# Performance work log

Hardware: AMD Instinct MI355X
Metric: run time of the kernel (lower is better)

## Reference

```python
import jax, jax.numpy as jnp
import numpy as np

N = 100000      # nodes
E = 1600000     # edges (before self-loops)
IN_DIM = 128
HEADS1, C1 = 8, 16   # conv1: hidden_dim=16, heads=8 -> 128 concat
OUT_DIM = 40
NEG_SLOPE = 0.2


def setup_inputs() -> dict:
    key = jax.random.key(0)
    ks = jax.random.split(key, 10)
    s = 0.1
    x = jax.random.normal(ks[0], (N, IN_DIM), dtype=jnp.float32)
    edge_index = jax.random.randint(ks[1], (2, E), 0, N)
    W1 = jax.random.normal(ks[2], (IN_DIM, HEADS1 * C1), dtype=jnp.float32) * s
    att_l1 = jax.random.normal(ks[3], (HEADS1, C1), dtype=jnp.float32) * s
    att_r1 = jax.random.normal(ks[4], (HEADS1, C1), dtype=jnp.float32) * s
    b1 = jnp.zeros((HEADS1 * C1,), dtype=jnp.float32)
    W2 = jax.random.normal(ks[5], (HEADS1 * C1, OUT_DIM), dtype=jnp.float32) * s
    att_l2 = jax.random.normal(ks[6], (1, OUT_DIM), dtype=jnp.float32) * s
    att_r2 = jax.random.normal(ks[7], (1, OUT_DIM), dtype=jnp.float32) * s
    b2 = jnp.zeros((OUT_DIM,), dtype=jnp.float32)
    return {"x": x, "edge_index": edge_index, "W1": W1, "att_l1": att_l1,
            "att_r1": att_r1, "b1": b1, "W2": W2, "att_l2": att_l2,
            "att_r2": att_r2, "b2": b2}


def supergat_layer(x, src, dst, W, att_l, att_r, bias, concat):
    """One SuperGATConv layer, MX attention, inference mode (no dropout)."""
    n = x.shape[0]
    heads, out_ch = att_l.shape
    h = (x @ W).reshape(n, heads, out_ch)      # [N, H, C]
    h_i = h[dst]                               # target features  [E2, H, C]
    h_j = h[src]                               # source features  [E2, H, C]
    # MX attention: mix of GO (learned att vectors) gated by DP (dot product)
    logits = jnp.sum(h_i * h_j, axis=-1)                           # [E2, H]
    alpha = jnp.sum(h_j * att_l, axis=-1) + jnp.sum(h_i * att_r, axis=-1)
    alpha = alpha * jax.nn.sigmoid(logits)
    alpha = jax.nn.leaky_relu(alpha, NEG_SLOPE)
    # segment softmax over destination node (every node has a self-loop)
    a_max = jax.ops.segment_max(alpha, dst, num_segments=n)        # [N, H]
    ex = jnp.exp(alpha - a_max[dst])
    denom = jax.ops.segment_sum(ex, dst, num_segments=n)           # [N, H]
    a = ex / denom[dst]                                            # [E2, H]
    out = jax.ops.segment_sum(h_j * a[..., None], dst, num_segments=n)  # [N,H,C]
    if concat:
        out = out.reshape(n, heads * out_ch)
    else:
        out = out.mean(axis=1)
    return out + bias


def reference(x, edge_index, W1, att_l1, att_r1, b1, W2, att_l2, att_r2, b2):
    n = x.shape[0]
    loops = jnp.arange(n, dtype=edge_index.dtype)
    ei = jnp.concatenate([edge_index, jnp.stack([loops, loops])], axis=1)
    src, dst = ei[0], ei[1]
    h = supergat_layer(x, src, dst, W1, att_l1, att_r1, b1, concat=True)
    h = jax.nn.elu(h)
    out = supergat_layer(h, src, dst, W2, att_l2, att_r2, b2, concat=False)
    return jax.nn.log_softmax(out, axis=1)
```

## Files before the change

kernel.cpp:

```cpp
#include <hip/hip_runtime.h>
#include <math.h>

#define N_NODES 100000
#define N_EDGES 1600000
#define E2 (N_EDGES + N_NODES)
#define NEG_SLOPE 0.2f

#define NPB 256
#define NB  ((N_NODES + NPB - 1) / NPB)
#define CAP 4800
#define BCH 8192

typedef unsigned int uint;
typedef unsigned short ushort;
typedef __attribute__((ext_vector_type(2))) _Float16 h2_t;
typedef __attribute__((ext_vector_type(8))) _Float16 f16x8;
typedef __attribute__((ext_vector_type(4))) float f32x4;

union U8 { uint4 q; f16x8 v; h2_t h2[4]; _Float16 h[8]; uint u[4]; };


__device__ inline ushort f2h(float x) {
  _Float16 h = (_Float16)x;
  return *(ushort*)&h;
}

__device__ inline float h2f(ushort u) {
  _Float16 h = *(_Float16*)&u;
  return (float)h;
}

__device__ inline h2_t pk2h(float a, float b) {
  auto r = __builtin_amdgcn_cvt_pkrtz(a, b);
  return *(h2_t*)&r;
}

__device__ inline float fdot2(h2_t a, h2_t b, float c) {
#if __has_builtin(__builtin_amdgcn_fdot2)
  return __builtin_amdgcn_fdot2(*(__fp16 __attribute__((ext_vector_type(2)))*)&a,
                                *(__fp16 __attribute__((ext_vector_type(2)))*)&b,
                                c, false);
#else
  return c + (float)a.x * (float)b.x + (float)a.y * (float)b.y;
#endif
}


__global__ __launch_bounds__(256) void k_prepW(const float* __restrict__ W1,
                                               const float* __restrict__ W2,
                                               ushort* __restrict__ WT1,
                                               ushort* __restrict__ WT2,
                                               int* __restrict__ bcursor) {
  int b = blockIdx.x, t = threadIdx.x;
  if (b == 0) {
    for (int i = t; i < 128 * 128; i += 256) {
      int k = i >> 7, n = i & 127;
      WT1[n * 128 + k] = f2h(W1[i]);
    }
  } else if (b == 1) {
    for (int i = t; i < 48 * 128; i += 256) {
      int n = i >> 7, k = i & 127;
      WT2[i] = (n < 40) ? f2h(W2[k * 40 + n]) : (ushort)0;
    }
  } else {
    for (int i = t; i < NB; i += 256) bcursor[i] = i * CAP;
  }
}


__global__ __launch_bounds__(256) void k_bucket(const int* __restrict__ ei,
                                                int* __restrict__ bcursor,
                                                uint* __restrict__ pbuf) {
  __shared__ int cnt[NB];
  __shared__ int base[NB];
  const int tid = threadIdx.x;
  const int ebase = blockIdx.x * BCH;
  for (int t = tid; t < NB; t += 256) cnt[t] = 0;
  __syncthreads();
#pragma unroll 4
  for (int k = 0; k < BCH / 256; ++k) {
    int e = ebase + tid + k * 256;
    if (e < E2) {
      int d = (e < N_EDGES) ? ei[N_EDGES + e] : (e - N_EDGES);
      atomicAdd(&cnt[d >> 8], 1);
    }
  }
  __syncthreads();
  for (int t = tid; t < NB; t += 256) {
    int c = cnt[t];
    base[t] = c ? atomicAdd(&bcursor[t], c) : 0;
    cnt[t] = 0;
  }
  __syncthreads();
#pragma unroll 4
  for (int k = 0; k < BCH / 256; ++k) {
    int e = ebase + tid + k * 256;
    if (e < E2) {
      int s, d;
      if (e < N_EDGES) { s = ei[e]; d = ei[N_EDGES + e]; }
      else { s = e - N_EDGES; d = s; }
      int b = d >> 8;
      int pos = base[b] + atomicAdd(&cnt[b], 1);
      pbuf[pos] = ((uint)s << 8) | (uint)(d & 255);
    }
  }
}

__global__ __launch_bounds__(512) void k_scanB(const int* __restrict__ bcursor,
                                               int* __restrict__ bbase,
                                               int* __restrict__ rowptr) {
  __shared__ int sm[512];
  int t = threadIdx.x;
  int v = (t < NB) ? (bcursor[t] - t * CAP) : 0;
  sm[t] = v;
  __syncthreads();
  for (int off = 1; off < 512; off <<= 1) {
    int u = (t >= off) ? sm[t - off] : 0;
    __syncthreads();
    sm[t] += u;
    __syncthreads();
  }
  if (t < NB) bbase[t] = sm[t] - v;
  if (t == 0) rowptr[N_NODES] = E2;
}

__global__ __launch_bounds__(256) void k_csr(const uint* __restrict__ pbuf,
                                             const int* __restrict__ bcursor,
                                             const int* __restrict__ bbase,
                                             int* __restrict__ rowptr,
                                             int* __restrict__ csr) {
  __shared__ int hist[NPB];
  __shared__ int excl[NPB];
  __shared__ int cur[NPB];
  __shared__ int lcsr[CAP];
  const int b = blockIdx.x;
  const int tid = threadIdx.x;
  int count = bcursor[b] - b * CAP;
  if (count > CAP) count = CAP;
  const int gbase = bbase[b];
  const uint* seg = pbuf + b * CAP;
  hist[tid] = 0;
  __syncthreads();
  for (int k = tid; k < count; k += 256) atomicAdd(&hist[seg[k] & 255u], 1);
  __syncthreads();
  int own = hist[tid];
  excl[tid] = own;
  __syncthreads();
  for (int off = 1; off < 256; off <<= 1) {
    int u = (tid >= off) ? excl[tid - off] : 0;
    __syncthreads();
    excl[tid] += u;
    __syncthreads();
  }
  int ex = excl[tid] - own;
  cur[tid] = ex;
  int node = b * NPB + tid;
  if (node < N_NODES) rowptr[node] = gbase + ex;
  __syncthreads();
  for (int k = tid; k < count; k += 256) {
    uint pk = seg[k];
    int nd = pk & 255u;
    int pos = atomicAdd(&cur[nd], 1);
    lcsr[pos] = (int)(pk >> 8);
  }
  __syncthreads();
  for (int k = tid; k < count; k += 256) csr[gbase + k] = lcsr[k];
}


__global__ __launch_bounds__(256) void k_gemm1m(const float* __restrict__ x,
                                                const ushort* __restrict__ WT1,
                                                const float* __restrict__ attl,
                                                const float* __restrict__ attr,
                                                ushort* __restrict__ h1h,
                                                ushort* __restrict__ al1h,
                                                float* __restrict__ ar1) {
  __shared__ ushort stg[4][16][136];
  __shared__ h2_t attl_sm[64], attr_sm[64];
  const int tid = threadIdx.x;
  const int w = tid >> 6, l = tid & 63;
  const int r16 = l & 15, kq = l >> 4;
  const int rowbase = blockIdx.x * 64 + w * 16;
  if (tid < 64) attl_sm[tid] = pk2h(attl[2 * tid], attl[2 * tid + 1]);
  else if (tid < 128) { int t = tid - 64; attr_sm[t] = pk2h(attr[2 * t], attr[2 * t + 1]); }
  int arow = rowbase + r16;
  if (arow > N_NODES - 1) arow = N_NODES - 1;
  f16x8 af[4];
  const float* xr = x + (size_t)arow * 128 + kq * 8;
#pragma unroll
  for (int t = 0; t < 4; ++t) {
    float4 a0 = *(const float4*)(xr + t * 32);
    float4 a1 = *(const float4*)(xr + t * 32 + 4);
    U8 u;
    u.h2[0] = pk2h(a0.x, a0.y); u.h2[1] = pk2h(a0.z, a0.w);
    u.h2[2] = pk2h(a1.x, a1.y); u.h2[3] = pk2h(a1.z, a1.w);
    af[t] = u.v;
  }
  f32x4 acc[8];
#pragma unroll
  for (int n = 0; n < 8; ++n) acc[n] = (f32x4){0.f, 0.f, 0.f, 0.f};
  const uint4* WT4 = (const uint4*)WT1;
#pragma unroll
  for (int t = 0; t < 4; ++t) {
#pragma unroll
    for (int n = 0; n < 8; ++n) {
      U8 b;
      b.q = WT4[(size_t)(n * 16 + r16) * 16 + t * 4 + kq];
      acc[n] = __builtin_amdgcn_mfma_f32_16x16x32_f16(af[t], b.v, acc[n], 0, 0, 0);
    }
  }
#pragma unroll
  for (int n = 0; n < 8; ++n) {
#pragma unroll
    for (int r = 0; r < 4; ++r) stg[w][kq * 4 + r][n * 16 + r16] = f2h(acc[n][r]);
  }
  __syncthreads();
  uint4* H1 = (uint4*)h1h;
  const uint4* S = (const uint4*)stg[w];
#pragma unroll
  for (int q = 0; q < 4; ++q) {
    int idx = l + q * 64;
    int row = idx >> 4, c4 = idx & 15;
    int grow = rowbase + row;
    if (grow < N_NODES) H1[(size_t)grow * 16 + c4] = S[row * 17 + c4];
  }
#pragma unroll
  for (int p = 0; p < 2; ++p) {
    int pidx = l + p * 64;
    int row = pidx >> 3, h = pidx & 7;
    int grow = rowbase + row;
    U8 a0, a1;
    a0.q = S[row * 17 + h * 2];
    a1.q = S[row * 17 + h * 2 + 1];
    float sl = 0.f, sr = 0.f;
#pragma unroll
    for (int k = 0; k < 4; ++k) {
      sl = fdot2(a0.h2[k], attl_sm[h * 8 + k], sl);
      sr = fdot2(a0.h2[k], attr_sm[h * 8 + k], sr);
      sl = fdot2(a1.h2[k], attl_sm[h * 8 + 4 + k], sl);
      sr = fdot2(a1.h2[k], attr_sm[h * 8 + 4 + k], sr);
    }
    if (grow < N_NODES) {
      al1h[(size_t)grow * 8 + h] = f2h(sl);
      ar1[(size_t)grow * 8 + h] = sr;
    }
  }
}


__global__ __launch_bounds__(256) void k_edge1(const ushort* __restrict__ h1h,
                                               const ushort* __restrict__ al1h,
                                               const float* __restrict__ ar1,
                                               const int* __restrict__ rowptr,
                                               const int* __restrict__ csr,
                                               const float* __restrict__ b1,
                                               ushort* __restrict__ y1h) {
  const int tid = threadIdx.x;
  const int lane = tid & 63;
  const int wv = tid >> 6;
  const int grp = lane >> 4;
  const int l = lane & 15;
  const int h = l >> 1;
  const int node0 = (blockIdx.x * 4 + wv) * 4 + grp;
  const bool alive = node0 < N_NODES;
  const int i = alive ? node0 : N_NODES - 1;
  const int start = rowptr[i], end = rowptr[i + 1];
  const uint4* H = (const uint4*)h1h;
  U8 uhi;
  uhi.q = H[(size_t)i * 16 + l];
  const float ar_i = ar1[i * 8 + h];
  float s = 0.f;
  float acc[8] = {};
  for (int e = start; e < end; e += 4) {
    int e1 = e + 1 < end ? e + 1 : end - 1;
    int e2 = e + 2 < end ? e + 2 : end - 1;
    int e3 = e + 3 < end ? e + 3 : end - 1;
    int j0 = csr[e], j1 = csr[e1], j2 = csr[e2], j3 = csr[e3];
    U8 u0, u1, u2, u3;
    u0.q = H[(size_t)j0 * 16 + l];
    u1.q = H[(size_t)j1 * 16 + l];
    u2.q = H[(size_t)j2 * 16 + l];
    u3.q = H[(size_t)j3 * 16 + l];
    float al0 = h2f(al1h[j0 * 8 + h]);
    float al1 = h2f(al1h[j1 * 8 + h]);
    float al2 = h2f(al1h[j2 * 8 + h]);
    float al3 = h2f(al1h[j3 * 8 + h]);
    float p0 = 0.f, p1 = 0.f, p2 = 0.f, p3 = 0.f;
#pragma unroll
    for (int k = 0; k < 4; ++k) {
      p0 = fdot2(uhi.h2[k], u0.h2[k], p0);
      p1 = fdot2(uhi.h2[k], u1.h2[k], p1);
      p2 = fdot2(uhi.h2[k], u2.h2[k], p2);
      p3 = fdot2(uhi.h2[k], u3.h2[k], p3);
    }
    p0 += __shfl_xor(p0, 1);
    p1 += __shfl_xor(p1, 1);
    p2 += __shfl_xor(p2, 1);
    p3 += __shfl_xor(p3, 1);
    float a0 = (al0 + ar_i) * (1.f / (1.f + __expf(-p0)));
    float a1 = (al1 + ar_i) * (1.f / (1.f + __expf(-p1)));
    float a2 = (al2 + ar_i) * (1.f / (1.f + __expf(-p2)));
    float a3 = (al3 + ar_i) * (1.f / (1.f + __expf(-p3)));
    a0 = fmaxf(a0, NEG_SLOPE * a0);
    a1 = fmaxf(a1, NEG_SLOPE * a1);
    a2 = fmaxf(a2, NEG_SLOPE * a2);
    a3 = fmaxf(a3, NEG_SLOPE * a3);
    float ex0 = __expf(a0);
    float ex1 = (e + 1 < end) ? __expf(a1) : 0.f;
    float ex2 = (e + 2 < end) ? __expf(a2) : 0.f;
    float ex3 = (e + 3 < end) ? __expf(a3) : 0.f;
    s += (ex0 + ex1) + (ex2 + ex3);
#pragma unroll
    for (int c = 0; c < 8; ++c) {
      float t0 = fmaf(ex0, (float)u0.h[c], ex1 * (float)u1.h[c]);
      float t1 = fmaf(ex2, (float)u2.h[c], ex3 * (float)u3.h[c]);
      acc[c] += t0 + t1;
    }
  }
  float inv = 1.f / s;
  float4 bb0 = *(const float4*)(b1 + l * 8);
  float4 bb1 = *(const float4*)(b1 + l * 8 + 4);
  float o[8];
  o[0] = acc[0] * inv + bb0.x; o[1] = acc[1] * inv + bb0.y;
  o[2] = acc[2] * inv + bb0.z; o[3] = acc[3] * inv + bb0.w;
  o[4] = acc[4] * inv + bb1.x; o[5] = acc[5] * inv + bb1.y;
  o[6] = acc[6] * inv + bb1.z; o[7] = acc[7] * inv + bb1.w;
#pragma unroll
  for (int c = 0; c < 8; ++c) o[c] = o[c] > 0.f ? o[c] : __expf(o[c]) - 1.f;
  if (alive) {
    U8 pk;
#pragma unroll
    for (int c = 0; c < 4; ++c) pk.h2[c] = pk2h(o[2 * c], o[2 * c + 1]);
    ((uint4*)y1h)[(size_t)i * 16 + l] = pk.q;
  }
}


__global__ __launch_bounds__(256) void k_gemm2m(const ushort* __restrict__ y1h,
                                                const ushort* __restrict__ WT2,
                                                const float* __restrict__ attl,
                                                const float* __restrict__ attr,
                                                ushort* __restrict__ h2p,
                                                float* __restrict__ al2,
                                                float* __restrict__ ar2) {
  __shared__ ushort stg[4][16][56];
  __shared__ h2_t attl_sm[20], attr_sm[20];
  const int tid = threadIdx.x;
  const int w = tid >> 6, l = tid & 63;
  const int r16 = l & 15, kq = l >> 4;
  const int rowbase = blockIdx.x * 64 + w * 16;
  if (tid < 20) attl_sm[tid] = pk2h(attl[2 * tid], attl[2 * tid + 1]);
  else if (tid >= 32 && tid < 52) { int t = tid - 32; attr_sm[t] = pk2h(attr[2 * t], attr[2 * t + 1]); }
  int arow = rowbase + r16;
  if (arow > N_NODES - 1) arow = N_NODES - 1;
  const uint4* Y4 = (const uint4*)y1h;
  f16x8 af[4];
#pragma unroll
  for (int t = 0; t < 4; ++t) {
    U8 u;
    u.q = Y4[(size_t)arow * 16 + t * 4 + kq];
    af[t] = u.v;
  }
  f32x4 acc[3];
#pragma unroll
  for (int n = 0; n < 3; ++n) acc[n] = (f32x4){0.f, 0.f, 0.f, 0.f};
  const uint4* WT4 = (const uint4*)WT2;
#pragma unroll
  for (int t = 0; t < 4; ++t) {
#pragma unroll
    for (int n = 0; n < 3; ++n) {
      U8 b;
      b.q = WT4[(size_t)(n * 16 + r16) * 16 + t * 4 + kq];
      acc[n] = __builtin_amdgcn_mfma_f32_16x16x32_f16(af[t], b.v, acc[n], 0, 0, 0);
    }
  }
#pragma unroll
  for (int n = 0; n < 3; ++n) {
#pragma unroll
    for (int r = 0; r < 4; ++r) stg[w][kq * 4 + r][n * 16 + r16] = f2h(acc[n][r]);
  }
  __syncthreads();
  uint4* H2 = (uint4*)h2p;
  const uint4* S = (const uint4*)stg[w];
  const uint4 z = make_uint4(0, 0, 0, 0);
#pragma unroll
  for (int q = 0; q < 2; ++q) {
    int idx = l + q * 64;
    int row = idx >> 3, c4 = idx & 7;
    int grow = rowbase + row;
    if (grow < N_NODES) H2[(size_t)grow * 8 + c4] = (c4 < 6) ? S[row * 7 + c4] : z;
  }
  if (l < 32) {
    int row = l & 15, sel = l >> 4;
    int grow = rowbase + row;
    const h2_t* att = sel ? attr_sm : attl_sm;
    float v = 0.f;
#pragma unroll
    for (int q = 0; q < 5; ++q) {
      U8 b;
      b.q = S[row * 7 + q];
#pragma unroll
      for (int k = 0; k < 4; ++k) v = fdot2(b.h2[k], att[q * 4 + k], v);
    }
    if (grow < N_NODES) {
      if (sel) ar2[grow] = v;
      else     al2[grow] = v;
    }
  }
}


__global__ __launch_bounds__(256) void k_edge2(const ushort* __restrict__ h2p,
                                               const float* __restrict__ al,
                                               const float* __restrict__ ar,
                                               const int* __restrict__ rowptr,
                                               const int* __restrict__ csr,
                                               const float* __restrict__ b2,
                                               float* __restrict__ out) {
  const int tid = threadIdx.x;
  const int lane = tid & 63;
  const int wv = tid >> 6;
  const int grp = lane >> 3;
  const int l = lane & 7;
  const int node0 = (blockIdx.x * 4 + wv) * 8 + grp;
  const bool alive = node0 < N_NODES;
  const int i = alive ? node0 : N_NODES - 1;
  const int start = rowptr[i], end = rowptr[i + 1];
  const uint4* H = (const uint4*)h2p;
  U8 uhi;
  uhi.q = H[(size_t)i * 8 + l];
  const float ar_i = ar[i];
  float s = 0.f;
  float acc[8] = {};
  for (int e = start; e < end; e += 4) {
    int e1 = e + 1 < end ? e + 1 : end - 1;
    int e2 = e + 2 < end ? e + 2 : end - 1;
    int e3 = e + 3 < end ? e + 3 : end - 1;
    int j0 = csr[e], j1 = csr[e1], j2 = csr[e2], j3 = csr[e3];
    U8 u0, u1, u2, u3;
    u0.q = H[(size_t)j0 * 8 + l];
    u1.q = H[(size_t)j1 * 8 + l];
    u2.q = H[(size_t)j2 * 8 + l];
    u3.q = H[(size_t)j3 * 8 + l];
    float al0 = al[j0], al1 = al[j1], al2 = al[j2], al3 = al[j3];
    float p0 = 0.f, p1 = 0.f, p2 = 0.f, p3 = 0.f;
#pragma unroll
    for (int k = 0; k < 4; ++k) {
      p0 = fdot2(uhi.h2[k], u0.h2[k], p0);
      p1 = fdot2(uhi.h2[k], u1.h2[k], p1);
      p2 = fdot2(uhi.h2[k], u2.h2[k], p2);
      p3 = fdot2(uhi.h2[k], u3.h2[k], p3);
    }
#pragma unroll
    for (int m = 1; m <= 4; m <<= 1) {
      p0 += __shfl_xor(p0, m);
      p1 += __shfl_xor(p1, m);
      p2 += __shfl_xor(p2, m);
      p3 += __shfl_xor(p3, m);
    }
    float a0 = (al0 + ar_i) * (1.f / (1.f + __expf(-p0)));
    float a1 = (al1 + ar_i) * (1.f / (1.f + __expf(-p1)));
    float a2 = (al2 + ar_i) * (1.f / (1.f + __expf(-p2)));
    float a3 = (al3 + ar_i) * (1.f / (1.f + __expf(-p3)));
    a0 = fmaxf(a0, NEG_SLOPE * a0);
    a1 = fmaxf(a1, NEG_SLOPE * a1);
    a2 = fmaxf(a2, NEG_SLOPE * a2);
    a3 = fmaxf(a3, NEG_SLOPE * a3);
    float ex0 = __expf(a0);
    float ex1 = (e + 1 < end) ? __expf(a1) : 0.f;
    float ex2 = (e + 2 < end) ? __expf(a2) : 0.f;
    float ex3 = (e + 3 < end) ? __expf(a3) : 0.f;
    s += (ex0 + ex1) + (ex2 + ex3);
#pragma unroll
    for (int c = 0; c < 8; ++c) {
      float t0 = fmaf(ex0, (float)u0.h[c], ex1 * (float)u1.h[c]);
      float t1 = fmaf(ex2, (float)u2.h[c], ex3 * (float)u3.h[c]);
      acc[c] += t0 + t1;
    }
  }
  float inv = 1.f / s;
  bool act = l < 5;
  float o[8];
  float mx = -1e30f;
#pragma unroll
  for (int c = 0; c < 8; ++c) {
    float b = act ? b2[l * 8 + c] : 0.f;
    o[c] = acc[c] * inv + b;
    if (act) mx = fmaxf(mx, o[c]);
  }
  mx = fmaxf(mx, __shfl_xor(mx, 1));
  mx = fmaxf(mx, __shfl_xor(mx, 2));
  mx = fmaxf(mx, __shfl_xor(mx, 4));
  float se = 0.f;
  if (act) {
#pragma unroll
    for (int c = 0; c < 8; ++c) se += __expf(o[c] - mx);
  }
  se += __shfl_xor(se, 1);
  se += __shfl_xor(se, 2);
  se += __shfl_xor(se, 4);
  if (alive && act) {
    float lse = mx + __logf(se);
    float4 r0 = make_float4(o[0] - lse, o[1] - lse, o[2] - lse, o[3] - lse);
    float4 r1 = make_float4(o[4] - lse, o[5] - lse, o[6] - lse, o[7] - lse);
    float4* O = (float4*)(out + (size_t)i * 40 + l * 8);
    O[0] = r0;
    O[1] = r1;
  }
}


extern "C" void kernel_launch(void* const* d_in, const int* in_sizes, int n_in,
                              void* d_out, int out_size, void* d_ws, size_t ws_size,
                              hipStream_t stream) {
  const float* x     = (const float*)d_in[0];
  const int*   ei    = (const int*)d_in[1];
  const float* W1    = (const float*)d_in[2];
  const float* attl1 = (const float*)d_in[3];
  const float* attr1 = (const float*)d_in[4];
  const float* b1    = (const float*)d_in[5];
  const float* W2    = (const float*)d_in[6];
  const float* attl2 = (const float*)d_in[7];
  const float* attr2 = (const float*)d_in[8];
  const float* b2    = (const float*)d_in[9];
  float* out = (float*)d_out;

  char* wsp = (char*)d_ws;
  size_t off = 0;
  auto alloc = [&](size_t bytes) {
    char* p = wsp + off;
    off = (off + bytes + 255) & ~(size_t)255;
    return p;
  };
  ushort* h1h   = (ushort*)alloc((size_t)N_NODES * 128 * 2);
  ushort* y1h   = (ushort*)alloc((size_t)N_NODES * 128 * 2);
  ushort* al1h  = (ushort*)alloc((size_t)N_NODES * 8 * 2);
  float* ar1    = (float*)alloc((size_t)N_NODES * 8 * 4);
  int* rowptr   = (int*)alloc((size_t)(N_NODES + 1) * 4);
  int* bcursor  = (int*)alloc((size_t)NB * 4);
  int* bbase    = (int*)alloc((size_t)NB * 4);
  int* csr      = (int*)alloc((size_t)E2 * 4);
  ushort* WT1   = (ushort*)alloc(128 * 128 * 2);
  ushort* WT2   = (ushort*)alloc(48 * 128 * 2);
  uint* pbuf  = (uint*)y1h;
  ushort* h2p = h1h;
  float* al2  = (float*)ar1;
  float* ar2  = al2 + N_NODES;

  k_prepW<<<3, 256, 0, stream>>>(W1, W2, WT1, WT2, bcursor);
  k_bucket<<<(E2 + BCH - 1) / BCH, 256, 0, stream>>>(ei, bcursor, pbuf);
  k_scanB<<<1, 512, 0, stream>>>(bcursor, bbase, rowptr);
  k_csr<<<NB, 256, 0, stream>>>(pbuf, bcursor, bbase, rowptr, csr);

  k_gemm1m<<<(N_NODES + 63) / 64, 256, 0, stream>>>(x, WT1, attl1, attr1, h1h, al1h, ar1);
  k_edge1<<<(N_NODES + 15) / 16, 256, 0, stream>>>(h1h, al1h, ar1, rowptr, csr, b1, y1h);

  k_gemm2m<<<(N_NODES + 63) / 64, 256, 0, stream>>>(y1h, WT2, attl2, attr2, h2p, al2, ar2);
  k_edge2<<<(N_NODES + 31) / 32, 256, 0, stream>>>(h2p, al2, ar2, rowptr, csr, b2, out);
}
```

Baseline: 251.9 us.

## Pad CSR rows to multiples of four with sentinel node, fp16 accumulation, compact layer-2 rows

Each node's CSR row is padded to a multiple of 4 entries, filled with a sentinel node index N whose features are zero and whose attention logit is -inf. Per-row start/end arrays replace rowptr, so the edge loops can load four neighbour indices with one int4 and drop the tail clamping and masking. The weighted feature accumulation moves from fp32 scalar FMAs to packed fp16 vector multiply-adds. Layer-2 features are stored at 80 bytes per row instead of 128, which cuts gather traffic but risks fp16 accumulation error and adds padding edges to process.

```diff
diff --git a/kernel.cpp b/kernel.cpp
--- a/kernel.cpp
+++ b/kernel.cpp
@@ -9,6 +9,8 @@
 #define NPB 256
 #define NB  ((N_NODES + NPB - 1) / NPB)
 #define CAP 4800
+#define CAPP (CAP + 3 * NPB)
+#define BSLACK 772
 #define BCH 8192
 
 typedef unsigned int uint;
@@ -107,8 +109,7 @@
 }
 
 __global__ __launch_bounds__(512) void k_scanB(const int* __restrict__ bcursor,
-                                               int* __restrict__ bbase,
-                                               int* __restrict__ rowptr) {
+                                               int* __restrict__ bbase) {
   __shared__ int sm[512];
   int t = threadIdx.x;
   int v = (t < NB) ? (bcursor[t] - t * CAP) : 0;
@@ -120,19 +121,22 @@
     sm[t] += u;
     __syncthreads();
   }
-  if (t < NB) bbase[t] = sm[t] - v;
-  if (t == 0) rowptr[N_NODES] = E2;
+  if (t < NB) {
+    int excl = sm[t] - v;
+    bbase[t] = ((excl + 3) & ~3) + t * BSLACK;
+  }
 }
 
 __global__ __launch_bounds__(256) void k_csr(const uint* __restrict__ pbuf,
                                              const int* __restrict__ bcursor,
                                              const int* __restrict__ bbase,
-                                             int* __restrict__ rowptr,
+                                             int* __restrict__ rs,
+                                             int* __restrict__ re,
                                              int* __restrict__ csr) {
   __shared__ int hist[NPB];
   __shared__ int excl[NPB];
   __shared__ int cur[NPB];
-  __shared__ int lcsr[CAP];
+  __shared__ int lcsr[CAPP];
   const int b = blockIdx.x;
   const int tid = threadIdx.x;
   int count = bcursor[b] - b * CAP;
@@ -143,8 +147,8 @@
   __syncthreads();
   for (int k = tid; k < count; k += 256) atomicAdd(&hist[seg[k] & 255u], 1);
   __syncthreads();
-  int own = hist[tid];
-  excl[tid] = own;
+  int rounded = (hist[tid] + 3) & ~3;
+  excl[tid] = rounded;
   __syncthreads();
   for (int off = 1; off < 256; off <<= 1) {
     int u = (tid >= off) ? excl[tid - off] : 0;
@@ -152,10 +156,16 @@
     excl[tid] += u;
     __syncthreads();
   }
-  int ex = excl[tid] - own;
+  int ex = excl[tid] - rounded;
   cur[tid] = ex;
   int node = b * NPB + tid;
-  if (node < N_NODES) rowptr[node] = gbase + ex;
+  if (node < N_NODES) {
+    rs[node] = gbase + ex;
+    re[node] = gbase + ex + rounded;
+  }
+  __syncthreads();
+  const int ptotal = excl[NPB - 1];
+  for (int k = tid; k < ptotal; k += 256) lcsr[k] = N_NODES;
   __syncthreads();
   for (int k = tid; k < count; k += 256) {
     uint pk = seg[k];
@@ -164,7 +174,7 @@
     lcsr[pos] = (int)(pk >> 8);
   }
   __syncthreads();
-  for (int k = tid; k < count; k += 256) csr[gbase + k] = lcsr[k];
+  for (int k = tid; k < ptotal; k += 256) csr[gbase + k] = lcsr[k];
 }
 
 
@@ -183,6 +193,10 @@
   const int rowbase = blockIdx.x * 64 + w * 16;
   if (tid < 64) attl_sm[tid] = pk2h(attl[2 * tid], attl[2 * tid + 1]);
   else if (tid < 128) { int t = tid - 64; attr_sm[t] = pk2h(attr[2 * t], attr[2 * t + 1]); }
+  if (blockIdx.x == 0) {
+    if (tid >= 128 && tid < 144) ((uint4*)h1h)[(size_t)N_NODES * 16 + (tid - 128)] = make_uint4(0, 0, 0, 0);
+    else if (tid >= 144 && tid < 152) al1h[(size_t)N_NODES * 8 + (tid - 144)] = (ushort)0xFC00;
+  }
   int arow = rowbase + r16;
   if (arow > N_NODES - 1) arow = N_NODES - 1;
   f16x8 af[4];
@@ -249,9 +263,10 @@
 
 
 __global__ __launch_bounds__(256) void k_edge1(const ushort* __restrict__ h1h,
-                                               const ushort* __restrict__ al1h,
+                                               const ushort* __restrict__ alT,
                                                const float* __restrict__ ar1,
-                                               const int* __restrict__ rowptr,
+                                               const int* __restrict__ rs,
+                                               const int* __restrict__ re,
                                                const int* __restrict__ csr,
                                                const float* __restrict__ b1,
                                                ushort* __restrict__ y1h) {
@@ -264,27 +279,28 @@
   const int node0 = (blockIdx.x * 4 + wv) * 4 + grp;
   const bool alive = node0 < N_NODES;
   const int i = alive ? node0 : N_NODES - 1;
-  const int start = rowptr[i], end = rowptr[i + 1];
-  const uint4* H = (const uint4*)h1h;
+  const int start = rs[i], end = re[i];
+  const char* Hb = (const char*)h1h;
+  const char* Ab = (const char*)alT;
+  const char* Cb = (const char*)csr;
+  const uint loff = (uint)l * 16u;
+  const uint aoff = (uint)h * 2u;
   U8 uhi;
-  uhi.q = H[(size_t)i * 16 + l];
+  uhi.q = *(const uint4*)(Hb + (uint)i * 256u + loff);
   const float ar_i = ar1[i * 8 + h];
   float s = 0.f;
-  float acc[8] = {};
+  f16x8 acc = {};
   for (int e = start; e < end; e += 4) {
-    int e1 = e + 1 < end ? e + 1 : end - 1;
-    int e2 = e + 2 < end ? e + 2 : end - 1;
-    int e3 = e + 3 < end ? e + 3 : end - 1;
-    int j0 = csr[e], j1 = csr[e1], j2 = csr[e2], j3 = csr[e3];
+    int4 j4 = *(const int4*)(Cb + (uint)e * 4u);
     U8 u0, u1, u2, u3;
-    u0.q = H[(size_t)j0 * 16 + l];
-    u1.q = H[(size_t)j1 * 16 + l];
-    u2.q = H[(size_t)j2 * 16 + l];
-    u3.q = H[(size_t)j3 * 16 + l];
-    float al0 = h2f(al1h[j0 * 8 + h]);
-    float al1 = h2f(al1h[j1 * 8 + h]);
-    float al2 = h2f(al1h[j2 * 8 + h]);
-    float al3 = h2f(al1h[j3 * 8 + h]);
+    u0.q = *(const uint4*)(Hb + (uint)j4.x * 256u + loff);
+    u1.q = *(const uint4*)(Hb + (uint)j4.y * 256u + loff);
+    u2.q = *(const uint4*)(Hb + (uint)j4.z * 256u + loff);
+    u3.q = *(const uint4*)(Hb + (uint)j4.w * 256u + loff);
+    float av0 = h2f(*(const ushort*)(Ab + (uint)j4.x * 16u + aoff));
+    float av1 = h2f(*(const ushort*)(Ab + (uint)j4.y * 16u + aoff));
+    float av2 = h2f(*(const ushort*)(Ab + (uint)j4.z * 16u + aoff));
+    float av3 = h2f(*(const ushort*)(Ab + (uint)j4.w * 16u + aoff));
     float p0 = 0.f, p1 = 0.f, p2 = 0.f, p3 = 0.f;
 #pragma unroll
     for (int k = 0; k < 4; ++k) {
@@ -297,36 +313,34 @@
     p1 += __shfl_xor(p1, 1);
     p2 += __shfl_xor(p2, 1);
     p3 += __shfl_xor(p3, 1);
-    float a0 = (al0 + ar_i) * (1.f / (1.f + __expf(-p0)));
-    float a1 = (al1 + ar_i) * (1.f / (1.f + __expf(-p1)));
-    float a2 = (al2 + ar_i) * (1.f / (1.f + __expf(-p2)));
-    float a3 = (al3 + ar_i) * (1.f / (1.f + __expf(-p3)));
+    float a0 = (av0 + ar_i) * (1.f / (1.f + __expf(-p0)));
+    float a1 = (av1 + ar_i) * (1.f / (1.f + __expf(-p1)));
+    float a2 = (av2 + ar_i) * (1.f / (1.f + __expf(-p2)));
+    float a3 = (av3 + ar_i) * (1.f / (1.f + __expf(-p3)));
     a0 = fmaxf(a0, NEG_SLOPE * a0);
     a1 = fmaxf(a1, NEG_SLOPE * a1);
     a2 = fmaxf(a2, NEG_SLOPE * a2);
     a3 = fmaxf(a3, NEG_SLOPE * a3);
     float ex0 = __expf(a0);
-    float ex1 = (e + 1 < end) ? __expf(a1) : 0.f;
-    float ex2 = (e + 2 < end) ? __expf(a2) : 0.f;
-    float ex3 = (e + 3 < end) ? __expf(a3) : 0.f;
+    float ex1 = __expf(a1);
+    float ex2 = __expf(a2);
+    float ex3 = __expf(a3);
     s += (ex0 + ex1) + (ex2 + ex3);
-#pragma unroll
-    for (int c = 0; c < 8; ++c) {
-      float t0 = fmaf(ex0, (float)u0.h[c], ex1 * (float)u1.h[c]);
-      float t1 = fmaf(ex2, (float)u2.h[c], ex3 * (float)u3.h[c]);
-      acc[c] += t0 + t1;
-    }
+    acc += u0.v * (_Float16)ex0;
+    acc += u1.v * (_Float16)ex1;
+    acc += u2.v * (_Float16)ex2;
+    acc += u3.v * (_Float16)ex3;
   }
   float inv = 1.f / s;
   float4 bb0 = *(const float4*)(b1 + l * 8);
   float4 bb1 = *(const float4*)(b1 + l * 8 + 4);
   float o[8];
-  o[0] = acc[0] * inv + bb0.x; o[1] = acc[1] * inv + bb0.y;
-  o[2] = acc[2] * inv + bb0.z; o[3] = acc[3] * inv + bb0.w;
-  o[4] = acc[4] * inv + bb1.x; o[5] = acc[5] * inv + bb1.y;
-  o[6] = acc[6] * inv + bb1.z; o[7] = acc[7] * inv + bb1.w;
-#pragma unroll
-  for (int c = 0; c < 8; ++c) o[c] = o[c] > 0.f ? o[c] : __expf(o[c]) - 1.f;
+#pragma unroll
+  for (int c = 0; c < 8; ++c) {
+    float b = (c < 4) ? ((const float*)&bb0)[c] : ((const float*)&bb1)[c - 4];
+    float v = (float)acc[c] * inv + b;
+    o[c] = v > 0.f ? v : __expf(v) - 1.f;
+  }
   if (alive) {
     U8 pk;
 #pragma unroll
@@ -351,6 +365,10 @@
   const int rowbase = blockIdx.x * 64 + w * 16;
   if (tid < 20) attl_sm[tid] = pk2h(attl[2 * tid], attl[2 * tid + 1]);
   else if (tid >= 32 && tid < 52) { int t = tid - 32; attr_sm[t] = pk2h(attr[2 * t], attr[2 * t + 1]); }
+  if (blockIdx.x == 0) {
+    if (tid >= 64 && tid < 69) ((uint4*)h2p)[(size_t)N_NODES * 5 + (tid - 64)] = make_uint4(0, 0, 0, 0);
+    else if (tid == 69) al2[N_NODES] = -INFINITY;
+  }
   int arow = rowbase + r16;
   if (arow > N_NODES - 1) arow = N_NODES - 1;
   const uint4* Y4 = (const uint4*)y1h;
@@ -382,13 +400,14 @@
   __syncthreads();
   uint4* H2 = (uint4*)h2p;
   const uint4* S = (const uint4*)stg[w];
-  const uint4 z = make_uint4(0, 0, 0, 0);
 #pragma unroll
   for (int q = 0; q < 2; ++q) {
     int idx = l + q * 64;
-    int row = idx >> 3, c4 = idx & 7;
-    int grow = rowbase + row;
-    if (grow < N_NODES) H2[(size_t)grow * 8 + c4] = (c4 < 6) ? S[row * 7 + c4] : z;
+    if (idx < 80) {
+      int row = idx / 5, c4 = idx % 5;
+      int grow = rowbase + row;
+      if (grow < N_NODES) H2[(size_t)grow * 5 + c4] = S[row * 7 + c4];
+    }
   }
   if (l < 32) {
     int row = l & 15, sel = l >> 4;
@@ -411,9 +430,10 @@
 
 
 __global__ __launch_bounds__(256) void k_edge2(const ushort* __restrict__ h2p,
-                                               const float* __restrict__ al,
-                                               const float* __restrict__ ar,
-                                               const int* __restrict__ rowptr,
+                                               const float* __restrict__ alT,
+                                               const float* __restrict__ ar2,
+                                               const int* __restrict__ rs,
+                                               const int* __restrict__ re,
                                                const int* __restrict__ csr,
                                                const float* __restrict__ b2,
                                                float* __restrict__ out) {
@@ -425,24 +445,27 @@
   const int node0 = (blockIdx.x * 4 + wv) * 8 + grp;
   const bool alive = node0 < N_NODES;
   const int i = alive ? node0 : N_NODES - 1;
-  const int start = rowptr[i], end = rowptr[i + 1];
-  const uint4* H = (const uint4*)h2p;
+  const int start = rs[i], end = re[i];
+  const char* Hb = (const char*)h2p;
+  const char* Cb = (const char*)csr;
+  const uint loff = (uint)(l < 5 ? l : 0) * 16u;
   U8 uhi;
-  uhi.q = H[(size_t)i * 8 + l];
-  const float ar_i = ar[i];
+  uhi.q = *(const uint4*)(Hb + (uint)i * 80u + loff);
+  if (l >= 5) uhi.q = make_uint4(0, 0, 0, 0);
+  const float ar_i = ar2[i];
   float s = 0.f;
-  float acc[8] = {};
+  f16x8 acc = {};
   for (int e = start; e < end; e += 4) {
-    int e1 = e + 1 < end ? e + 1 : end - 1;
-    int e2 = e + 2 < end ? e + 2 : end - 1;
-    int e3 = e + 3 < end ? e + 3 : end - 1;
-    int j0 = csr[e], j1 = csr[e1], j2 = csr[e2], j3 = csr[e3];
+    int4 j4 = *(const int4*)(Cb + (uint)e * 4u);
     U8 u0, u1, u2, u3;
-    u0.q = H[(size_t)j0 * 8 + l];
-    u1.q = H[(size_t)j1 * 8 + l];
-    u2.q = H[(size_t)j2 * 8 + l];
-    u3.q = H[(size_t)j3 * 8 + l];
-    float al0 = al[j0], al1 = al[j1], al2 = al[j2], al3 = al[j3];
+    u0.q = *(const uint4*)(Hb + (uint)j4.x * 80u + loff);
+    u1.q = *(const uint4*)(Hb + (uint)j4.y * 80u + loff);
+    u2.q = *(const uint4*)(Hb + (uint)j4.z * 80u + loff);
+    u3.q = *(const uint4*)(Hb + (uint)j4.w * 80u + loff);
+    float av0 = alT[j4.x];
+    float av1 = alT[j4.y];
+    float av2 = alT[j4.z];
+    float av3 = alT[j4.w];
     float p0 = 0.f, p1 = 0.f, p2 = 0.f, p3 = 0.f;
 #pragma unroll
     for (int k = 0; k < 4; ++k) {
@@ -458,25 +481,23 @@
       p2 += __shfl_xor(p2, m);
       p3 += __shfl_xor(p3, m);
     }
-    float a0 = (al0 + ar_i) * (1.f / (1.f + __expf(-p0)));
-    float a1 = (al1 + ar_i) * (1.f / (1.f + __expf(-p1)));
-    float a2 = (al2 + ar_i) * (1.f / (1.f + __expf(-p2)));
-    float a3 = (al3 + ar_i) * (1.f / (1.f + __expf(-p3)));
+    float a0 = (av0 + ar_i) * (1.f / (1.f + __expf(-p0)));
+    float a1 = (av1 + ar_i) * (1.f / (1.f + __expf(-p1)));
+    float a2 = (av2 + ar_i) * (1.f / (1.f + __expf(-p2)));
+    float a3 = (av3 + ar_i) * (1.f / (1.f + __expf(-p3)));
     a0 = fmaxf(a0, NEG_SLOPE * a0);
     a1 = fmaxf(a1, NEG_SLOPE * a1);
     a2 = fmaxf(a2, NEG_SLOPE * a2);
     a3 = fmaxf(a3, NEG_SLOPE * a3);
     float ex0 = __expf(a0);
-    float ex1 = (e + 1 < end) ? __expf(a1) : 0.f;
-    float ex2 = (e + 2 < end) ? __expf(a2) : 0.f;
-    float ex3 = (e + 3 < end) ? __expf(a3) : 0.f;
+    float ex1 = __expf(a1);
+    float ex2 = __expf(a2);
+    float ex3 = __expf(a3);
     s += (ex0 + ex1) + (ex2 + ex3);
-#pragma unroll
-    for (int c = 0; c < 8; ++c) {
-      float t0 = fmaf(ex0, (float)u0.h[c], ex1 * (float)u1.h[c]);
-      float t1 = fmaf(ex2, (float)u2.h[c], ex3 * (float)u3.h[c]);
-      acc[c] += t0 + t1;
-    }
+    acc += u0.v * (_Float16)ex0;
+    acc += u1.v * (_Float16)ex1;
+    acc += u2.v * (_Float16)ex2;
+    acc += u3.v * (_Float16)ex3;
   }
   float inv = 1.f / s;
   bool act = l < 5;
@@ -485,7 +506,7 @@
 #pragma unroll
   for (int c = 0; c < 8; ++c) {
     float b = act ? b2[l * 8 + c] : 0.f;
-    o[c] = acc[c] * inv + b;
+    o[c] = (float)acc[c] * inv + b;
     if (act) mx = fmaxf(mx, o[c]);
   }
   mx = fmaxf(mx, __shfl_xor(mx, 1));
@@ -532,29 +553,30 @@
     off = (off + bytes + 255) & ~(size_t)255;
     return p;
   };
-  ushort* h1h   = (ushort*)alloc((size_t)N_NODES * 128 * 2);
+  ushort* h1h   = (ushort*)alloc((size_t)(N_NODES + 1) * 128 * 2);
   ushort* y1h   = (ushort*)alloc((size_t)N_NODES * 128 * 2);
-  ushort* al1h  = (ushort*)alloc((size_t)N_NODES * 8 * 2);
+  ushort* al1h  = (ushort*)alloc((size_t)(N_NODES + 1) * 8 * 2);
   float* ar1    = (float*)alloc((size_t)N_NODES * 8 * 4);
-  int* rowptr   = (int*)alloc((size_t)(N_NODES + 1) * 4);
+  int* rs       = (int*)alloc((size_t)(N_NODES + 4) * 4);
+  int* re       = (int*)alloc((size_t)(N_NODES + 4) * 4);
   int* bcursor  = (int*)alloc((size_t)NB * 4);
   int* bbase    = (int*)alloc((size_t)NB * 4);
-  int* csr      = (int*)alloc((size_t)E2 * 4);
+  int* csr      = (int*)alloc((size_t)(E2 + NB * BSLACK + 16) * 4);
   ushort* WT1   = (ushort*)alloc(128 * 128 * 2);
   ushort* WT2   = (ushort*)alloc(48 * 128 * 2);
   uint* pbuf  = (uint*)y1h;
   ushort* h2p = h1h;
   float* al2  = (float*)ar1;
-  float* ar2  = al2 + N_NODES;
+  float* ar2  = al2 + N_NODES + 8;
 
   k_prepW<<<3, 256, 0, stream>>>(W1, W2, WT1, WT2, bcursor);
   k_bucket<<<(E2 + BCH - 1) / BCH, 256, 0, stream>>>(ei, bcursor, pbuf);
-  k_scanB<<<1, 512, 0, stream>>>(bcursor, bbase, rowptr);
-  k_csr<<<NB, 256, 0, stream>>>(pbuf, bcursor, bbase, rowptr, csr);
+  k_scanB<<<1, 512, 0, stream>>>(bcursor, bbase);
+  k_csr<<<NB, 256, 0, stream>>>(pbuf, bcursor, bbase, rs, re, csr);
 
   k_gemm1m<<<(N_NODES + 63) / 64, 256, 0, stream>>>(x, WT1, attl1, attr1, h1h, al1h, ar1);
-  k_edge1<<<(N_NODES + 15) / 16, 256, 0, stream>>>(h1h, al1h, ar1, rowptr, csr, b1, y1h);
+  k_edge1<<<(N_NODES + 15) / 16, 256, 0, stream>>>(h1h, al1h, ar1, rs, re, csr, b1, y1h);
 
   k_gemm2m<<<(N_NODES + 63) / 64, 256, 0, stream>>>(y1h, WT2, attl2, attr2, h2p, al2, ar2);
-  k_edge2<<<(N_NODES + 31) / 32, 256, 0, stream>>>(h2p, al2, ar2, rowptr, csr, b2, out);
-}
+  k_edge2<<<(N_NODES + 31) / 32, 256, 0, stream>>>(h2p, al2, ar2, rs, re, csr, b2, out);
+}
```

New measurement: 232.6 us. -7.6%, faster.
